# Kernel optimization log

Measured on AMD Instinct MI355X. Metric: run time of the kernel, lower is better.

The kernel has to match this reference:

```python
import jax, jax.numpy as jnp
import numpy as np

B, C, T = 128, 16, 2048
H = 256            # hidden_size
G = 4 * H          # gate dim (i, f, g, o in torch order)
NUM_OUT = 10


def setup_inputs() -> dict:
    key = jax.random.key(0)
    ks = jax.random.split(key, 7)
    s = 1.0 / np.sqrt(H)  # torch default LSTM init scale
    return {
        "x": jax.random.normal(ks[0], (B, C, T), dtype=jnp.float32),
        "w_ih": jax.random.uniform(ks[1], (G, C), minval=-s, maxval=s, dtype=jnp.float32),
        "w_hh": jax.random.uniform(ks[2], (G, H), minval=-s, maxval=s, dtype=jnp.float32),
        "b_ih": jax.random.uniform(ks[3], (G,), minval=-s, maxval=s, dtype=jnp.float32),
        "b_hh": jax.random.uniform(ks[4], (G,), minval=-s, maxval=s, dtype=jnp.float32),
        "w_out": jax.random.uniform(ks[5], (NUM_OUT, H), minval=-s, maxval=s, dtype=jnp.float32),
        "b_out": jax.random.uniform(ks[6], (NUM_OUT,), minval=-s, maxval=s, dtype=jnp.float32),
    }


def _lstm_last_hidden(x, w_ih, w_hh, b_ih, b_hh):
    # x: (B, C, T) -> (B, T, C)
    xt = jnp.swapaxes(x, 1, 2)
    # Precompute input projections for all timesteps: (B, T, 4H)
    xproj = jnp.einsum('btc,gc->btg', xt, w_ih) + b_ih + b_hh
    xs = jnp.swapaxes(xproj, 0, 1)  # (T, B, 4H) for scan

    h0 = jnp.zeros((xt.shape[0], w_hh.shape[1]), dtype=x.dtype)
    c0 = jnp.zeros_like(h0)

    def step(carry, xp):
        h, cell = carry
        gates = xp + h @ w_hh.T               # (B, 4H)
        i, f, g, o = jnp.split(gates, 4, axis=-1)  # torch gate order i,f,g,o
        i = jax.nn.sigmoid(i)
        f = jax.nn.sigmoid(f)
        g = jnp.tanh(g)
        o = jax.nn.sigmoid(o)
        cell = f * cell + i * g
        h = o * jnp.tanh(cell)
        return (h, cell), None

    (hT, _), _ = jax.lax.scan(step, (h0, c0), xs)
    return hT  # (B, H): hidden state at last timestep


def reference(x, w_ih, w_hh, b_ih, b_hh, w_out, b_out):
    # bn0 is Identity (c.normalize_data=True)
    hT = _lstm_last_hidden(x, w_ih, w_hh, b_ih, b_hh)
    logits = hT @ w_out.T + b_out  # (B, num_outputs)
    return jax.nn.log_softmax(logits, axis=1)
```

## Files before the change

### kernel.cpp

```cpp
#include <hip/hip_runtime.h>
#include <cstdint>
#include <cstddef>

#define NB 128
#define NC 16
#define NT 2048
#define NH 256
#define NG 1024
#define NO 10

typedef _Float16 f16;
typedef _Float16 h2 __attribute__((ext_vector_type(2)));
typedef _Float16 h8 __attribute__((ext_vector_type(8)));
typedef int i32x4 __attribute__((ext_vector_type(4)));
typedef long long2_ __attribute__((ext_vector_type(2)));

static __device__ __forceinline__ float fdot2(h2 a, h2 b, float c) {
#if __has_builtin(__builtin_amdgcn_fdot2)
  return __builtin_amdgcn_fdot2(a, b, c, false);
#else
  return c + (float)a[0] * (float)b[0] + (float)a[1] * (float)b[1];
#endif
}

static __device__ __forceinline__ i32x4 mfma_i8_k64(i32x4 a, i32x4 b, i32x4 c) {
#if __has_builtin(__builtin_amdgcn_mfma_i32_16x16x64_i8)
  return __builtin_amdgcn_mfma_i32_16x16x64_i8(a, b, c, 0, 0, 0);
#else
  long2_ al = __builtin_bit_cast(long2_, a);
  long2_ bl = __builtin_bit_cast(long2_, b);
  c = __builtin_amdgcn_mfma_i32_16x16x32_i8(al[0], bl[0], c, 0, 0, 0);
  c = __builtin_amdgcn_mfma_i32_16x16x32_i8(al[1], bl[1], c, 0, 0, 0);
  return c;
#endif
}

static __device__ __forceinline__ float sigm(float x) {
  return __builtin_amdgcn_rcpf(1.f + __expf(-x));
}
static __device__ __forceinline__ float tanh_(float x) {
  return 1.f - 2.f * __builtin_amdgcn_rcpf(1.f + __expf(2.f * x));
}

__global__ void prepack_whh_i8(const float* __restrict__ whh,
                               int8_t* __restrict__ wq,
                               float* __restrict__ scale) {
  int row = blockIdx.x;
  int k   = threadIdx.x;
  float v = whh[row * NH + k];
  float m = fabsf(v);
  for (int off = 32; off; off >>= 1) m = fmaxf(m, __shfl_xor(m, off, 64));
  __shared__ float smax[4];
  if ((k & 63) == 0) smax[k >> 6] = m;
  __syncthreads();
  float mm = fmaxf(fmaxf(smax[0], smax[1]), fmaxf(smax[2], smax[3]));
  float s = fmaxf(mm, 1e-20f) / 127.f;
  int qv = (int)rintf(v / s);
  qv = min(127, max(-127, qv));
  wq[row * NH + k] = (int8_t)qv;
  if (k == 0) scale[row] = s;
}

__global__ __launch_bounds__(512, 2)
void lstm_main(const float* __restrict__ x,
               const float* __restrict__ w_ih,
               const float* __restrict__ b_ih,
               const float* __restrict__ b_hh,
               const float* __restrict__ w_out,
               const float* __restrict__ b_out,
               const int8_t* __restrict__ wq,
               const float* __restrict__ scales,
               float* __restrict__ out) {
  const int t = threadIdx.x;
  const int l = t & 63;
  const int w = t >> 6;
  const int b = blockIdx.x;
  const int row16 = l & 15;
  const int grp = l >> 4;
  const int sel = grp & 1;
  const int uu = 32 * w + 16 * sel + row16;

  __shared__ __align__(16) int8_t hq[2][NH];
  __shared__ __align__(16) f16 xs[64][NC];
  __shared__ float hT[NH];
  __shared__ float lg[NO];

  i32x4 bw[4][2][4];
#pragma unroll
  for (int gt = 0; gt < 4; ++gt)
#pragma unroll
    for (int hf = 0; hf < 2; ++hf) {
      const int8_t* rp =
          wq + (size_t)(256 * gt + 32 * w + 16 * hf + row16) * NH + grp * 16;
#pragma unroll
      for (int kt = 0; kt < 4; ++kt)
        bw[gt][hf][kt] = *(const i32x4*)(rp + kt * 64);
    }

  h2 wih[4][8];
#pragma unroll
  for (int gt = 0; gt < 4; ++gt) {
    const float* rp = w_ih + (size_t)(256 * gt + uu) * NC;
#pragma unroll
    for (int q = 0; q < 8; ++q) {
      h2 t2 = {(f16)rp[2 * q], (f16)rp[2 * q + 1]};
      wih[gt][q] = t2;
    }
  }
  const float K = 1.f / 127.f;
  float sc[4], bb[4];
#pragma unroll
  for (int gt = 0; gt < 4; ++gt) {
    sc[gt] = scales[256 * gt + uu] * K;
    bb[gt] = b_ih[256 * gt + uu] + b_hh[256 * gt + uu];
  }

  ((int8_t*)hq)[t] = 0;
#pragma unroll
  for (int r = 0; r < 2; ++r) {
    int e = t + 512 * r;
    int cc = e >> 6, tt = e & 63;
    xs[tt][cc] = (f16)x[(size_t)(b * NC + cc) * NT + tt];
  }
  __syncthreads();

  float c_ = 0.f, h_last = 0.f;

#pragma unroll 1
  for (int s = 0; s < NT; ++s) {
    const int p = s & 1;

    const int8_t* hp = hq[p] + grp * 16;
    i32x4 a_[4];
#pragma unroll
    for (int kt = 0; kt < 4; ++kt) a_[kt] = *(const i32x4*)(hp + kt * 64);

    h8 xlo = *(const h8*)&xs[s & 63][0];
    h8 xhi = *(const h8*)&xs[s & 63][8];
    float xp[4];
#pragma unroll
    for (int gt = 0; gt < 4; ++gt) {
      float acc = bb[gt];
#pragma unroll
      for (int q = 0; q < 4; ++q) {
        h2 xa = {xlo[2 * q], xlo[2 * q + 1]};
        acc = fdot2(xa, wih[gt][q], acc);
      }
#pragma unroll
      for (int q = 0; q < 4; ++q) {
        h2 xa = {xhi[2 * q], xhi[2 * q + 1]};
        acc = fdot2(xa, wih[gt][q + 4], acc);
      }
      xp[gt] = acc;
    }

    i32x4 acc[4][2];
#pragma unroll
    for (int gt = 0; gt < 4; ++gt)
#pragma unroll
      for (int hf = 0; hf < 2; ++hf) {
        i32x4 ac = {0, 0, 0, 0};
#pragma unroll
        for (int kt = 0; kt < 4; ++kt)
          ac = mfma_i8_k64(a_[kt], bw[gt][hf][kt], ac);
        acc[gt][hf] = ac;
      }

    float gv[4];
#pragma unroll
    for (int gt = 0; gt < 4; ++gt) {
      int d = sel ? acc[gt][1][0] : acc[gt][0][0];
      gv[gt] = xp[gt] + (float)d * sc[gt];
    }

    float ig = sigm(gv[0]);
    float fg = sigm(gv[1]);
    float gg = tanh_(gv[2]);
    float og = sigm(gv[3]);
    c_ = fg * c_ + ig * gg;
    float hh = og * tanh_(c_);
    h_last = hh;
    if (l < 32) hq[1 - p][uu] = (int8_t)(int)rintf(hh * 127.f);

    if ((s & 63) == 63 && s != NT - 1) {
      __syncthreads();
#pragma unroll
      for (int r = 0; r < 2; ++r) {
        int e = t + 512 * r;
        int cc = e >> 6, tt = e & 63;
        xs[tt][cc] = (f16)x[(size_t)(b * NC + cc) * NT + (s + 1) + tt];
      }
    }
    __syncthreads();
  }

  if (l < 32) hT[uu] = h_last;
  __syncthreads();
  if (t < NO) {
    float acc = b_out[t];
    for (int k = 0; k < NH; ++k) acc += hT[k] * w_out[t * NH + k];
    lg[t] = acc;
  }
  __syncthreads();
  if (t == 0) {
    float m = lg[0];
    for (int o = 1; o < NO; ++o) m = fmaxf(m, lg[o]);
    float ssum = 0.f;
    for (int o = 0; o < NO; ++o) ssum += __expf(lg[o] - m);
    float lse = m + __logf(ssum);
    for (int o = 0; o < NO; ++o) out[b * NO + o] = lg[o] - lse;
  }
}

extern "C" void kernel_launch(void* const* d_in, const int* in_sizes, int n_in,
                              void* d_out, int out_size, void* d_ws, size_t ws_size,
                              hipStream_t stream) {
  const float* x    = (const float*)d_in[0];
  const float* wih  = (const float*)d_in[1];
  const float* whh  = (const float*)d_in[2];
  const float* bih  = (const float*)d_in[3];
  const float* bhh  = (const float*)d_in[4];
  const float* wout = (const float*)d_in[5];
  const float* bout = (const float*)d_in[6];
  float* out = (float*)d_out;
  int8_t* wq = (int8_t*)d_ws;
  float* scales = (float*)((char*)d_ws + NG * NH);

  hipLaunchKernelGGL(prepack_whh_i8, dim3(NG), dim3(NH), 0, stream, whh, wq, scales);
  hipLaunchKernelGGL(lstm_main, dim3(NB), dim3(512), 0, stream,
                     x, wih, bih, bhh, wout, bout, wq, scales, out);
}
```

Measured before the change: 1.862 ms.

## Split hidden units between MFMA waves and sdot4 VALU waves per step

```diff
diff --git a/kernel.cpp b/kernel.cpp
--- a/kernel.cpp
+++ b/kernel.cpp
@@ -20,6 +20,18 @@
   return __builtin_amdgcn_fdot2(a, b, c, false);
 #else
   return c + (float)a[0] * (float)b[0] + (float)a[1] * (float)b[1];
+#endif
+}
+
+static __device__ __forceinline__ int sdot4(int a, int b, int c) {
+#if __has_builtin(__builtin_amdgcn_sdot4)
+  return __builtin_amdgcn_sdot4(a, b, c, false);
+#else
+  int r = c;
+#pragma unroll
+  for (int i = 0; i < 4; ++i)
+    r += (int)(int8_t)(a >> (8 * i)) * (int)(int8_t)(b >> (8 * i));
+  return r;
 #endif
 }
 
@@ -33,6 +45,12 @@
   c = __builtin_amdgcn_mfma_i32_16x16x32_i8(al[1], bl[1], c, 0, 0, 0);
   return c;
 #endif
+}
+
+static __device__ __forceinline__ float pairswap(float v) {
+  int r = __builtin_amdgcn_update_dpp(0, __builtin_bit_cast(int, v),
+                                      0xB1, 0xF, 0xF, true);
+  return __builtin_bit_cast(float, r);
 }
 
 static __device__ __forceinline__ float sigm(float x) {
@@ -75,45 +93,11 @@
   const int l = t & 63;
   const int w = t >> 6;
   const int b = blockIdx.x;
-  const int row16 = l & 15;
-  const int grp = l >> 4;
-  const int sel = grp & 1;
-  const int uu = 32 * w + 16 * sel + row16;
 
   __shared__ __align__(16) int8_t hq[2][NH];
   __shared__ __align__(16) f16 xs[64][NC];
   __shared__ float hT[NH];
   __shared__ float lg[NO];
-
-  i32x4 bw[4][2][4];
-#pragma unroll
-  for (int gt = 0; gt < 4; ++gt)
-#pragma unroll
-    for (int hf = 0; hf < 2; ++hf) {
-      const int8_t* rp =
-          wq + (size_t)(256 * gt + 32 * w + 16 * hf + row16) * NH + grp * 16;
-#pragma unroll
-      for (int kt = 0; kt < 4; ++kt)
-        bw[gt][hf][kt] = *(const i32x4*)(rp + kt * 64);
-    }
-
-  h2 wih[4][8];
-#pragma unroll
-  for (int gt = 0; gt < 4; ++gt) {
-    const float* rp = w_ih + (size_t)(256 * gt + uu) * NC;
-#pragma unroll
-    for (int q = 0; q < 8; ++q) {
-      h2 t2 = {(f16)rp[2 * q], (f16)rp[2 * q + 1]};
-      wih[gt][q] = t2;
-    }
-  }
-  const float K = 1.f / 127.f;
-  float sc[4], bb[4];
-#pragma unroll
-  for (int gt = 0; gt < 4; ++gt) {
-    sc[gt] = scales[256 * gt + uu] * K;
-    bb[gt] = b_ih[256 * gt + uu] + b_hh[256 * gt + uu];
-  }
 
   ((int8_t*)hq)[t] = 0;
 #pragma unroll
@@ -124,77 +108,206 @@
   }
   __syncthreads();
 
-  float c_ = 0.f, h_last = 0.f;
-
+  const float K = 1.f / 127.f;
+
+  if (w < 4) {
+    const int row16 = l & 15;
+    const int grp = l >> 4;
+    const int sel = grp & 1;
+    const int uu = 32 * w + 16 * sel + row16;
+
+    i32x4 bw[4][2][4];
+#pragma unroll
+    for (int gt = 0; gt < 4; ++gt)
+#pragma unroll
+      for (int hf = 0; hf < 2; ++hf) {
+        const int8_t* rp =
+            wq + (size_t)(256 * gt + 32 * w + 16 * hf + row16) * NH + grp * 16;
+#pragma unroll
+        for (int kt = 0; kt < 4; ++kt)
+          bw[gt][hf][kt] = *(const i32x4*)(rp + kt * 64);
+      }
+
+    h2 wih[4][8];
+#pragma unroll
+    for (int gt = 0; gt < 4; ++gt) {
+      const float* rp = w_ih + (size_t)(256 * gt + uu) * NC;
+#pragma unroll
+      for (int q = 0; q < 8; ++q) {
+        h2 t2 = {(f16)rp[2 * q], (f16)rp[2 * q + 1]};
+        wih[gt][q] = t2;
+      }
+    }
+    float sc[4], bb[4];
+#pragma unroll
+    for (int gt = 0; gt < 4; ++gt) {
+      sc[gt] = scales[256 * gt + uu] * K;
+      bb[gt] = b_ih[256 * gt + uu] + b_hh[256 * gt + uu];
+    }
+
+    float c_ = 0.f, h_last = 0.f;
 #pragma unroll 1
-  for (int s = 0; s < NT; ++s) {
-    const int p = s & 1;
-
-    const int8_t* hp = hq[p] + grp * 16;
-    i32x4 a_[4];
-#pragma unroll
-    for (int kt = 0; kt < 4; ++kt) a_[kt] = *(const i32x4*)(hp + kt * 64);
-
-    h8 xlo = *(const h8*)&xs[s & 63][0];
-    h8 xhi = *(const h8*)&xs[s & 63][8];
-    float xp[4];
-#pragma unroll
-    for (int gt = 0; gt < 4; ++gt) {
-      float acc = bb[gt];
-#pragma unroll
-      for (int q = 0; q < 4; ++q) {
-        h2 xa = {xlo[2 * q], xlo[2 * q + 1]};
-        acc = fdot2(xa, wih[gt][q], acc);
-      }
-#pragma unroll
-      for (int q = 0; q < 4; ++q) {
-        h2 xa = {xhi[2 * q], xhi[2 * q + 1]};
-        acc = fdot2(xa, wih[gt][q + 4], acc);
-      }
-      xp[gt] = acc;
-    }
-
-    i32x4 acc[4][2];
-#pragma unroll
-    for (int gt = 0; gt < 4; ++gt)
-#pragma unroll
-      for (int hf = 0; hf < 2; ++hf) {
-        i32x4 ac = {0, 0, 0, 0};
-#pragma unroll
-        for (int kt = 0; kt < 4; ++kt)
-          ac = mfma_i8_k64(a_[kt], bw[gt][hf][kt], ac);
-        acc[gt][hf] = ac;
-      }
-
-    float gv[4];
-#pragma unroll
-    for (int gt = 0; gt < 4; ++gt) {
-      int d = sel ? acc[gt][1][0] : acc[gt][0][0];
-      gv[gt] = xp[gt] + (float)d * sc[gt];
-    }
-
-    float ig = sigm(gv[0]);
-    float fg = sigm(gv[1]);
-    float gg = tanh_(gv[2]);
-    float og = sigm(gv[3]);
-    c_ = fg * c_ + ig * gg;
-    float hh = og * tanh_(c_);
-    h_last = hh;
-    if (l < 32) hq[1 - p][uu] = (int8_t)(int)rintf(hh * 127.f);
-
-    if ((s & 63) == 63 && s != NT - 1) {
+    for (int s = 0; s < NT; ++s) {
+      const int p = s & 1;
+      const int8_t* hp = hq[p] + grp * 16;
+      i32x4 a_[4];
+#pragma unroll
+      for (int kt = 0; kt < 4; ++kt) a_[kt] = *(const i32x4*)(hp + kt * 64);
+
+      h8 xlo = *(const h8*)&xs[s & 63][0];
+      h8 xhi = *(const h8*)&xs[s & 63][8];
+      float xp[4];
+#pragma unroll
+      for (int gt = 0; gt < 4; ++gt) {
+        float acc = bb[gt];
+#pragma unroll
+        for (int q = 0; q < 4; ++q) {
+          h2 xa = {xlo[2 * q], xlo[2 * q + 1]};
+          acc = fdot2(xa, wih[gt][q], acc);
+        }
+#pragma unroll
+        for (int q = 0; q < 4; ++q) {
+          h2 xa = {xhi[2 * q], xhi[2 * q + 1]};
+          acc = fdot2(xa, wih[gt][q + 4], acc);
+        }
+        xp[gt] = acc;
+      }
+
+      float gv[4];
+#pragma unroll
+      for (int gt = 0; gt < 4; ++gt) {
+        i32x4 a0 = {0, 0, 0, 0}, a1 = {0, 0, 0, 0};
+#pragma unroll
+        for (int kt = 0; kt < 4; ++kt) a0 = mfma_i8_k64(a_[kt], bw[gt][0][kt], a0);
+#pragma unroll
+        for (int kt = 0; kt < 4; ++kt) a1 = mfma_i8_k64(a_[kt], bw[gt][1][kt], a1);
+        int d = sel ? a1[0] : a0[0];
+        gv[gt] = xp[gt] + (float)d * sc[gt];
+      }
+
+      float ig = sigm(gv[0]);
+      float fg = sigm(gv[1]);
+      float gg = tanh_(gv[2]);
+      float og = sigm(gv[3]);
+      c_ = fg * c_ + ig * gg;
+      float hh = og * tanh_(c_);
+      h_last = hh;
+      if (l < 32) hq[1 - p][uu] = (int8_t)(int)rintf(hh * 127.f);
+
+      if ((s & 63) == 63 && s != NT - 1) {
+        __syncthreads();
+#pragma unroll
+        for (int r = 0; r < 2; ++r) {
+          int e = t + 512 * r;
+          int cc = e >> 6, tt = e & 63;
+          xs[tt][cc] = (f16)x[(size_t)(b * NC + cc) * NT + (s + 1) + tt];
+        }
+      }
       __syncthreads();
-#pragma unroll
-      for (int r = 0; r < 2; ++r) {
-        int e = t + 512 * r;
-        int cc = e >> 6, tt = e & 63;
-        xs[tt][cc] = (f16)x[(size_t)(b * NC + cc) * NT + (s + 1) + tt];
-      }
-    }
-    __syncthreads();
+    }
+    if (l < 32) hT[uu] = h_last;
+  } else {
+    const int q = l >> 1;
+    const int half = l & 1;
+    const int uv = 128 + 32 * (w - 4) + q;
+
+    int wi_[32], wf_[32], wg_[32], wo_[32];
+    {
+      const int4* pi = (const int4*)(wq + (size_t)uv * NH + 128 * half);
+      const int4* pf = (const int4*)(wq + (size_t)(256 + uv) * NH + 128 * half);
+      const int4* pg = (const int4*)(wq + (size_t)(512 + uv) * NH + 128 * half);
+      const int4* po = (const int4*)(wq + (size_t)(768 + uv) * NH + 128 * half);
+#pragma unroll
+      for (int c = 0; c < 8; ++c) {
+        int4 vi = pi[c], vf = pf[c], vg = pg[c], vo = po[c];
+        wi_[4 * c + 0] = vi.x; wi_[4 * c + 1] = vi.y; wi_[4 * c + 2] = vi.z; wi_[4 * c + 3] = vi.w;
+        wf_[4 * c + 0] = vf.x; wf_[4 * c + 1] = vf.y; wf_[4 * c + 2] = vf.z; wf_[4 * c + 3] = vf.w;
+        wg_[4 * c + 0] = vg.x; wg_[4 * c + 1] = vg.y; wg_[4 * c + 2] = vg.z; wg_[4 * c + 3] = vg.w;
+        wo_[4 * c + 0] = vo.x; wo_[4 * c + 1] = vo.y; wo_[4 * c + 2] = vo.z; wo_[4 * c + 3] = vo.w;
+      }
+    }
+    h2 wihv[4][4];
+#pragma unroll
+    for (int g4 = 0; g4 < 4; ++g4) {
+      int row = uv + 256 * g4;
+#pragma unroll
+      for (int uu2 = 0; uu2 < 4; ++uu2) {
+        h2 t2 = {(f16)w_ih[row * NC + 8 * half + 2 * uu2],
+                 (f16)w_ih[row * NC + 8 * half + 2 * uu2 + 1]};
+        wihv[g4][uu2] = t2;
+      }
+    }
+    float sci = scales[uv] * K;
+    float scf = scales[256 + uv] * K;
+    float scg = scales[512 + uv] * K;
+    float sco = scales[768 + uv] * K;
+    float bi_ = half ? 0.f : b_ih[uv] + b_hh[uv];
+    float bf_ = half ? 0.f : b_ih[256 + uv] + b_hh[256 + uv];
+    float bg_ = half ? 0.f : b_ih[512 + uv] + b_hh[512 + uv];
+    float bo_ = half ? 0.f : b_ih[768 + uv] + b_hh[768 + uv];
+
+    float c_ = 0.f, h_last = 0.f;
+#pragma unroll 1
+    for (int s = 0; s < NT; ++s) {
+      const int p = s & 1;
+      const int4* hrd = (const int4*)(hq[p] + 128 * half);
+
+      float fi = bi_, ff = bf_, fg_ = bg_, fo = bo_;
+      {
+        h8 xv = *(const h8*)&xs[s & 63][8 * half];
+#pragma unroll
+        for (int uu2 = 0; uu2 < 4; ++uu2) {
+          h2 xp = {xv[2 * uu2], xv[2 * uu2 + 1]};
+          fi = fdot2(xp, wihv[0][uu2], fi);
+          ff = fdot2(xp, wihv[1][uu2], ff);
+          fg_ = fdot2(xp, wihv[2][uu2], fg_);
+          fo = fdot2(xp, wihv[3][uu2], fo);
+        }
+      }
+
+      int ai = 0, af = 0, ag = 0, ao = 0;
+#pragma unroll
+      for (int c = 0; c < 8; ++c) {
+        int4 hv = hrd[c];
+        ai = sdot4(hv.x, wi_[4 * c + 0], ai); ai = sdot4(hv.y, wi_[4 * c + 1], ai);
+        ai = sdot4(hv.z, wi_[4 * c + 2], ai); ai = sdot4(hv.w, wi_[4 * c + 3], ai);
+        af = sdot4(hv.x, wf_[4 * c + 0], af); af = sdot4(hv.y, wf_[4 * c + 1], af);
+        af = sdot4(hv.z, wf_[4 * c + 2], af); af = sdot4(hv.w, wf_[4 * c + 3], af);
+        ag = sdot4(hv.x, wg_[4 * c + 0], ag); ag = sdot4(hv.y, wg_[4 * c + 1], ag);
+        ag = sdot4(hv.z, wg_[4 * c + 2], ag); ag = sdot4(hv.w, wg_[4 * c + 3], ag);
+        ao = sdot4(hv.x, wo_[4 * c + 0], ao); ao = sdot4(hv.y, wo_[4 * c + 1], ao);
+        ao = sdot4(hv.z, wo_[4 * c + 2], ao); ao = sdot4(hv.w, wo_[4 * c + 3], ao);
+      }
+
+      float vi = fi + (float)ai * sci;
+      float vf = ff + (float)af * scf;
+      float vg = fg_ + (float)ag * scg;
+      float vo = fo + (float)ao * sco;
+      vi += pairswap(vi); vf += pairswap(vf); vg += pairswap(vg); vo += pairswap(vo);
+
+      float ig = sigm(vi);
+      float fgate = sigm(vf);
+      float gv = tanh_(vg);
+      float og = sigm(vo);
+      c_ = fgate * c_ + ig * gv;
+      float hh = og * tanh_(c_);
+      h_last = hh;
+      if (!half) hq[1 - p][uv] = (int8_t)(int)rintf(hh * 127.f);
+
+      if ((s & 63) == 63 && s != NT - 1) {
+        __syncthreads();
+#pragma unroll
+        for (int r = 0; r < 2; ++r) {
+          int e = t + 512 * r;
+          int cc = e >> 6, tt = e & 63;
+          xs[tt][cc] = (f16)x[(size_t)(b * NC + cc) * NT + (s + 1) + tt];
+        }
+      }
+      __syncthreads();
+    }
+    if (!half) hT[uv] = h_last;
   }
 
-  if (l < 32) hT[uu] = h_last;
   __syncthreads();
   if (t < NO) {
     float acc = b_out[t];
```

Measured after the change: 1.993 ms. 1.07x slower.
